# Performance work log

Hardware: AMD Instinct MI355X
Metric: run time of the kernel (lower is better)

The kernel has to match this reference:

```python
import jax, jax.numpy as jnp
import numpy as np

N, T, D, H, E, ED = 4096, 16, 5, 128, 32768, 32

def _leaky(x):
    return jnp.where(x >= 0, x, 0.2 * x)

def _lstm(x, Wih, Whh, bih, bhh):
    # x: [N, T, D] -> hidden sequence [N, T, H]; PyTorch gate order i,f,g,o
    pre = jnp.einsum('ntd,gd->tng', x, Wih) + bih + bhh  # [T, N, 4H]
    Hd = Whh.shape[1]
    def step(carry, p):
        h, c = carry
        g = p + h @ Whh.T
        i, f, gg, o = jnp.split(g, 4, axis=-1)
        c = jax.nn.sigmoid(f) * c + jax.nn.sigmoid(i) * jnp.tanh(gg)
        h = jax.nn.sigmoid(o) * jnp.tanh(c)
        return (h, c), h
    z = jnp.zeros((x.shape[0], Hd), x.dtype)
    _, hs = jax.lax.scan(step, (z, z), pre)
    return jnp.swapaxes(hs, 0, 1)

def _sire(x, src, dst, efeat, Wq, bq, Wk, bk, We, be, Wr, br):
    # SIREConv with agg_type='sum': m = LeakyReLU(eq[dst]+ek[src]+e); sum over in-edges; then linear_relation
    eq = x @ Wq.T + bq            # [N, T, H]
    ek = x @ Wk.T + bk            # [N, T, H]
    e = efeat @ We.T + be         # [E, H]
    m = _leaky(eq[dst] + ek[src] + e[:, None, :])  # [E, T, H]
    ft = jax.ops.segment_sum(m, dst, num_segments=x.shape[0])  # [N, T, H]
    return ft @ Wr.T + br

def _forward(stock_features, srcs, dsts, efeats, sire_ps, lstm_p, attn_p, mlp_p):
    sf = stock_features / jnp.mean(stock_features, axis=1, keepdims=True)
    sr = _lstm(sf, *lstm_p)  # [N, T, H]
    outs = [sr]
    for s, d, ef, p in zip(srcs, dsts, efeats, sire_ps):
        outs.append(_sire(sr, s, d, ef, *p))
    cat = jnp.concatenate(outs, axis=-1)  # [N, T, 4H]
    aw = jax.nn.softmax(cat @ attn_p[0].T + attn_p[1], axis=-2)  # softmax over time
    pooled = jnp.sum(cat * aw, axis=-2)   # [N, 4H]
    W1, b1, W2, b2 = mlp_p
    h = _leaky(pooled @ W1.T + b1)
    out = _leaky(h @ W2.T + b2)           # [N, 1]
    return out / sf[:, -1, 0:1] - 1.0


def setup_inputs() -> dict:
    key = jax.random.key(0)
    ks = iter(jax.random.split(key, 64))
    def nrm(shape, s=0.05):
        return jax.random.normal(next(ks), shape, jnp.float32) * s
    inp = {}
    inp['stock_features'] = jax.random.uniform(next(ks), (N, T, D), jnp.float32) + 0.5
    for g in ['wiki', 'industry', 'corr']:
        inp[g + '_src'] = jax.random.randint(next(ks), (E,), 0, N, jnp.int32)
        inp[g + '_dst'] = jax.random.randint(next(ks), (E,), 0, N, jnp.int32)
        inp[g + '_efeat'] = nrm((E, ED), 1.0)
        inp[g + '_Wq'] = nrm((H, H)); inp[g + '_bq'] = nrm((H,))
        inp[g + '_Wk'] = nrm((H, H)); inp[g + '_bk'] = nrm((H,))
        inp[g + '_We'] = nrm((H, ED)); inp[g + '_be'] = nrm((H,))
        inp[g + '_Wr'] = nrm((H, H)); inp[g + '_br'] = nrm((H,))
    inp['lstm_Wih'] = nrm((4 * H, D)); inp['lstm_Whh'] = nrm((4 * H, H))
    inp['lstm_bih'] = nrm((4 * H,)); inp['lstm_bhh'] = nrm((4 * H,))
    inp['attn_W'] = nrm((1, 4 * H)); inp['attn_b'] = nrm((1,))
    inp['mlp_W1'] = nrm((H, 4 * H)); inp['mlp_b1'] = nrm((H,))
    inp['mlp_W2'] = nrm((1, H)); inp['mlp_b2'] = nrm((1,))
    return inp


def reference(stock_features, wiki_src, wiki_dst, wiki_efeat,
              wiki_Wq, wiki_bq, wiki_Wk, wiki_bk, wiki_We, wiki_be, wiki_Wr, wiki_br,
              industry_src, industry_dst, industry_efeat,
              industry_Wq, industry_bq, industry_Wk, industry_bk, industry_We, industry_be, industry_Wr, industry_br,
              corr_src, corr_dst, corr_efeat,
              corr_Wq, corr_bq, corr_Wk, corr_bk, corr_We, corr_be, corr_Wr, corr_br,
              lstm_Wih, lstm_Whh, lstm_bih, lstm_bhh,
              attn_W, attn_b, mlp_W1, mlp_b1, mlp_W2, mlp_b2):
    srcs = (wiki_src, industry_src, corr_src)
    dsts = (wiki_dst, industry_dst, corr_dst)
    efeats = (wiki_efeat, industry_efeat, corr_efeat)
    sire_ps = ((wiki_Wq, wiki_bq, wiki_Wk, wiki_bk, wiki_We, wiki_be, wiki_Wr, wiki_br),
               (industry_Wq, industry_bq, industry_Wk, industry_bk, industry_We, industry_be, industry_Wr, industry_br),
               (corr_Wq, corr_bq, corr_Wk, corr_bk, corr_We, corr_be, corr_Wr, corr_br))
    return _forward(stock_features, srcs, dsts, efeats, sire_ps,
                    (lstm_Wih, lstm_Whh, lstm_bih, lstm_bhh),
                    (attn_W, attn_b), (mlp_W1, mlp_b1, mlp_W2, mlp_b2))
```

## Files before the change

### kernel.cpp

```cpp
#include <hip/hip_runtime.h>
#include <cstdint>
#include <cstddef>

#define NS 4096
#define TS 16
#define DF 5
#define HD 128
#define EE 32768
#define EDD 32

typedef __attribute__((ext_vector_type(8))) short bf16x8;
typedef __attribute__((ext_vector_type(4))) float f32x4;

__device__ __forceinline__ float sigmoidf_(float x){ return 1.f/(1.f+__expf(-x)); }
__device__ __forceinline__ float tanhf_(float x){ return 1.f - 2.f/(1.f+__expf(2.f*x)); }
__device__ __forceinline__ float leaky_(float x){ return x >= 0.f ? x : 0.2f*x; }

__device__ __forceinline__ unsigned short f2bf(float x){
  unsigned u = __float_as_uint(x);
  u += 0x7FFF + ((u>>16)&1);
  return (unsigned short)(u>>16);
}
__device__ __forceinline__ unsigned packbf(float a, float b){
  return (unsigned)f2bf(a) | ((unsigned)f2bf(b)<<16);
}
__device__ __forceinline__ void unpack2(unsigned u, float& a, float& b){
  a = __uint_as_float(u<<16);
  b = __uint_as_float(u & 0xFFFF0000u);
}
__device__ __forceinline__ void unpack8(uint4 q, float* f){
  unpack2(q.x, f[0], f[1]); unpack2(q.y, f[2], f[3]);
  unpack2(q.z, f[4], f[5]); unpack2(q.w, f[6], f[7]);
}
__device__ __forceinline__ bf16x8 ld_bf8(const unsigned short* p){
  union { uint4 u; bf16x8 v; } x; x.u = *(const uint4*)p; return x.v;
}

struct GemmB {
  const void* A[6];
  const float* B[6];
  const float* bias[6];
  void* C[6];
};
struct P3 { const int* p[3]; };

__global__ void k_sf(const float* __restrict__ x, float* __restrict__ sf){
  int id = blockIdx.x*256 + threadIdx.x;
  if (id >= NS*DF) return;
  int n = id / DF, d = id % DF;
  const float* xp = x + (size_t)n*TS*DF + d;
  float s = 0.f;
  #pragma unroll
  for (int t=0;t<TS;t++) s += xp[t*DF];
  float inv = (float)TS / s;
  float* sp = sf + (size_t)n*TS*DF + d;
  #pragma unroll
  for (int t=0;t<TS;t++) sp[t*DF] = xp[t*DF]*inv;
}

__global__ void k_cvt(const float* __restrict__ a, unsigned short* __restrict__ b, int n){
  int i = blockIdx.x*256 + threadIdx.x;
  if (i < n) b[i] = f2bf(a[i]);
}

__global__ __launch_bounds__(256,2)
void k_lstm(const float* __restrict__ sf, const unsigned short* __restrict__ WhhB,
            const float* __restrict__ Wih, const float* __restrict__ bih,
            const float* __restrict__ bhh, unsigned short* __restrict__ cat)
{
  __shared__ unsigned short hbuf[8*136];
  __shared__ float gates[8*516];
  __shared__ float sfb[8*80];
  int tid = threadIdx.x;
  int n0 = blockIdx.x * 8;
  int wv = tid>>6, lane = tid&63, lm = lane&15, lq = lane>>4;

  bf16x8 bfr[8][4];
  #pragma unroll
  for (int nt=0;nt<8;nt++){
    int g = wv*128 + nt*16 + lm;
    #pragma unroll
    for (int kt=0;kt<4;kt++)
      bfr[nt][kt] = *(const bf16x8*)&WhhB[g*128 + kt*32 + lq*8];
  }

  int j = tid & 127;
  int rbase = tid >> 7;
  float wih[4][5]; float bsum[4];
  #pragma unroll
  for (int gi=0; gi<4; gi++){
    int gc = gi*128 + j;
    #pragma unroll
    for (int d=0; d<5; d++) wih[gi][d] = Wih[gc*5+d];
    bsum[gi] = bih[gc] + bhh[gc];
  }
  float cst[4] = {0.f,0.f,0.f,0.f};

  for (int i=tid;i<8*136;i+=256) hbuf[i] = 0;
  for (int i=tid;i<8*80;i+=256) sfb[i] = sf[(size_t)n0*80 + i];
  __syncthreads();

  bf16x8 zf = {0,0,0,0,0,0,0,0};
  for (int t=0;t<16;t++){
    bf16x8 af[4];
    #pragma unroll
    for (int kt=0;kt<4;kt++)
      af[kt] = (lm < 8) ? *(const bf16x8*)&hbuf[lm*136 + kt*32 + lq*8] : zf;
    #pragma unroll
    for (int nt=0;nt<8;nt++){
      f32x4 acc = {0.f,0.f,0.f,0.f};
      #pragma unroll
      for (int kt=0;kt<4;kt++)
        acc = __builtin_amdgcn_mfma_f32_16x16x32_bf16(af[kt], bfr[nt][kt], acc, 0,0,0);
      if (lq < 2){
        int col = wv*128 + nt*16 + lm;
        #pragma unroll
        for (int i=0;i<4;i++)
          gates[(lq*4+i)*516 + col] = acc[i];
      }
    }
    __syncthreads();
    #pragma unroll
    for (int q=0;q<4;q++){
      int r = rbase + 2*q;
      const float* s = &sfb[r*80 + t*5];
      float pre[4];
      #pragma unroll
      for (int gi=0;gi<4;gi++){
        float a = bsum[gi];
        #pragma unroll
        for (int d=0;d<5;d++) a = fmaf(s[d], wih[gi][d], a);
        pre[gi] = a + gates[r*516 + gi*128 + j];
      }
      float iv = sigmoidf_(pre[0]);
      float fv = sigmoidf_(pre[1]);
      float gv = tanhf_(pre[2]);
      float ov = sigmoidf_(pre[3]);
      float c = fv*cst[q] + iv*gv;
      cst[q] = c;
      float h = ov*tanhf_(c);
      unsigned short hb = f2bf(h);
      hbuf[r*136 + j] = hb;
      cat[(size_t)((n0+r)*16 + t)*512 + j] = hb;
    }
    __syncthreads();
  }
}

template<int ABF, int CBF>
__global__ __launch_bounds__(256)
void gemm_mfma_b(GemmB gb, int lda, int ldb, int ldc, int K, int act)
{
  __shared__ unsigned short Asb[128*40];
  __shared__ unsigned short Bsb[128*40];
  int proj = blockIdx.x;
  size_t m0 = (size_t)blockIdx.y * 128;
  const float* Bp = gb.B[proj];
  const float* bp = gb.bias[proj];
  int tid = threadIdx.x;
  int wv = tid>>6, lane = tid&63, lm = lane&15, lq = lane>>4;

  f32x4 acc[2][8];
  #pragma unroll
  for (int mt=0;mt<2;mt++)
    #pragma unroll
    for (int nt=0;nt<8;nt++)
      acc[mt][nt] = (f32x4){0.f,0.f,0.f,0.f};

  for (int k0=0; k0<K; k0+=32){
    if (ABF){
      const unsigned short* A = (const unsigned short*)gb.A[proj];
      #pragma unroll
      for (int rep=0;rep<2;rep++){
        int idx = tid + rep*256;
        int row = idx>>2, c8 = idx&3;
        *(uint4*)&Asb[row*40 + c8*8] = *(const uint4*)&A[(m0+row)*(size_t)lda + k0 + c8*8];
      }
    } else {
      const float* A = (const float*)gb.A[proj];
      #pragma unroll
      for (int rep=0;rep<4;rep++){
        int idx = tid + rep*256;
        int row = idx>>3, c4 = idx&7;
        float4 a = *(const float4*)&A[(m0+row)*(size_t)lda + k0 + c4*4];
        *(uint2*)&Asb[row*40 + c4*4] = make_uint2(packbf(a.x,a.y), packbf(a.z,a.w));
      }
    }
    #pragma unroll
    for (int rep=0;rep<4;rep++){
      int idx = tid + rep*256;
      int row = idx>>3, c4 = idx&7;
      float4 b = *(const float4*)&Bp[(size_t)row*ldb + k0 + c4*4];
      *(uint2*)&Bsb[row*40 + c4*4] = make_uint2(packbf(b.x,b.y), packbf(b.z,b.w));
    }
    __syncthreads();
    bf16x8 afr[2], bfr[8];
    #pragma unroll
    for (int mt=0;mt<2;mt++)
      afr[mt] = ld_bf8(&Asb[(wv*32 + mt*16 + lm)*40 + lq*8]);
    #pragma unroll
    for (int nt=0;nt<8;nt++)
      bfr[nt] = ld_bf8(&Bsb[(nt*16 + lm)*40 + lq*8]);
    #pragma unroll
    for (int mt=0;mt<2;mt++)
      #pragma unroll
      for (int nt=0;nt<8;nt++)
        acc[mt][nt] = __builtin_amdgcn_mfma_f32_16x16x32_bf16(afr[mt], bfr[nt], acc[mt][nt], 0,0,0);
    __syncthreads();
  }

  #pragma unroll
  for (int mt=0;mt<2;mt++){
    #pragma unroll
    for (int nt=0;nt<8;nt++){
      int col = nt*16 + lm;
      float bv = bp[col];
      #pragma unroll
      for (int i=0;i<4;i++){
        float o = acc[mt][nt][i] + bv;
        if (act) o = leaky_(o);
        size_t ridx = (m0 + wv*32 + mt*16 + lq*4 + i)*(size_t)ldc + col;
        if (CBF) ((unsigned short*)gb.C[proj])[ridx] = f2bf(o);
        else     ((float*)gb.C[proj])[ridx] = o;
      }
    }
  }
}

__global__ void k_zero_i(int* p, int n){ int i=blockIdx.x*256+threadIdx.x; if(i<n) p[i]=0; }

__global__ void k_count(P3 dst, int* __restrict__ cnt){
  int e = blockIdx.x*256+threadIdx.x;
  int g = blockIdx.y;
  atomicAdd(&cnt[g*4096 + dst.p[g][e]], 1);
}

__global__ __launch_bounds__(1024)
void k_scan(const int* __restrict__ cnt_, int* __restrict__ rs_, int* __restrict__ woff_){
  __shared__ int buf[1024];
  int g = blockIdx.x;
  const int* cnt = cnt_ + g*4096;
  int* rs = rs_ + g*4097;
  int* woff = woff_ + g*4096;
  int tid = threadIdx.x;
  int b = tid*4;
  int v0=cnt[b],v1=cnt[b+1],v2=cnt[b+2],v3=cnt[b+3];
  int s = v0+v1+v2+v3;
  buf[tid]=s;
  __syncthreads();
  for (int off=1; off<1024; off<<=1){
    int t = (tid>=off) ? buf[tid-off] : 0;
    __syncthreads();
    buf[tid] += t;
    __syncthreads();
  }
  int excl = buf[tid] - s;
  rs[b+0]=excl; woff[b+0]=excl; excl+=v0;
  rs[b+1]=excl; woff[b+1]=excl; excl+=v1;
  rs[b+2]=excl; woff[b+2]=excl; excl+=v2;
  rs[b+3]=excl; woff[b+3]=excl;
  if (tid==1023) rs[4096]=excl+v3;
}

__global__ void k_fill(P3 dst, int* __restrict__ woff, int* __restrict__ eidx){
  int e = blockIdx.x*256+threadIdx.x;
  int g = blockIdx.y;
  int pos = atomicAdd(&woff[g*4096 + dst.p[g][e]], 1);
  eidx[g*EE + pos] = e;
}

__global__ __launch_bounds__(256)
void k_edge(const unsigned short* __restrict__ eqk, const unsigned short* __restrict__ eeb,
            P3 src, const int* __restrict__ rs_, const int* __restrict__ eidx_,
            unsigned short* __restrict__ ft_)
{
  int n = blockIdx.x;
  int g = blockIdx.y;
  const unsigned short* eqb = eqk + (size_t)(2*g)  *NS*TS*128;
  const unsigned short* ekb = eqk + (size_t)(2*g+1)*NS*TS*128;
  const unsigned short* eeg = eeb + (size_t)g*EE*128;
  unsigned short* ft = ft_ + (size_t)g*NS*TS*128;
  const int* srcp = src.p[g];
  const int* rs = rs_ + g*4097;
  const int* eidx = eidx_ + g*EE;
  int tid = threadIdx.x;
  int t = tid>>4, hb = (tid&15)*8;
  size_t own = ((size_t)(n*16+t))*128 + hb;
  float eqv[8], acc[8];
  unpack8(*(const uint4*)&eqb[own], eqv);
  #pragma unroll
  for (int j=0;j<8;j++) acc[j]=0.f;
  int i0 = rs[n], i1 = rs[n+1];
  for (int i=i0;i<i1;i++){
    int e = eidx[i];
    int s = srcp[e];
    uint4 kq = *(const uint4*)&ekb[((size_t)(s*16+t))*128 + hb];
    uint4 eq4 = *(const uint4*)&eeg[(size_t)e*128 + hb];
    float kf[8], ef[8];
    unpack8(kq, kf); unpack8(eq4, ef);
    #pragma unroll
    for (int j=0;j<8;j++)
      acc[j] += leaky_(eqv[j] + kf[j] + ef[j]);
  }
  uint4 o;
  o.x = packbf(acc[0],acc[1]); o.y = packbf(acc[2],acc[3]);
  o.z = packbf(acc[4],acc[5]); o.w = packbf(acc[6],acc[7]);
  *(uint4*)&ft[own] = o;
}

__global__ __launch_bounds__(256)
void k_attn(const unsigned short* __restrict__ cat, const float* __restrict__ attnW,
            const float* __restrict__ attnB, unsigned short* __restrict__ pooled)
{
  __shared__ unsigned short ct[16*512];
  __shared__ float sred[4][16];
  int n = blockIdx.x, tid = threadIdx.x;
  {
    const uint4* srcp = (const uint4*)(cat + (size_t)n*8192);
    uint4* dstp = (uint4*)ct;
    for (int i=tid;i<1024;i+=256) dstp[i] = srcp[i];
  }
  __syncthreads();
  int c0 = tid*2;
  float w0 = attnW[c0], w1 = attnW[c0+1];
  const unsigned* ctu = (const unsigned*)ct;
  float loc[16];
  #pragma unroll
  for (int t=0;t<16;t++){
    float a,b; unpack2(ctu[t*256 + tid], a, b);
    loc[t] = a*w0 + b*w1;
  }
  #pragma unroll
  for (int t=0;t<16;t++){
    float v = loc[t];
    for (int off=1; off<64; off<<=1) v += __shfl_xor(v, off, 64);
    loc[t]=v;
  }
  int wave = tid >> 6, lane = tid & 63;
  if (lane==0){
    #pragma unroll
    for (int t=0;t<16;t++) sred[wave][t]=loc[t];
  }
  __syncthreads();
  float s[16]; float m=-1e30f;
  float ab = attnB[0];
  #pragma unroll
  for (int t=0;t<16;t++){ s[t] = sred[0][t]+sred[1][t]+sred[2][t]+sred[3][t] + ab; m = fmaxf(m, s[t]); }
  float sum=0.f;
  #pragma unroll
  for (int t=0;t<16;t++){ s[t] = __expf(s[t]-m); sum += s[t]; }
  float inv = 1.f/sum;
  float p0=0.f,p1=0.f;
  #pragma unroll
  for (int t=0;t<16;t++){
    float a = s[t]*inv;
    float x,y; unpack2(ctu[t*256 + tid], x, y);
    p0 = fmaf(x, a, p0); p1 = fmaf(y, a, p1);
  }
  ((unsigned*)pooled)[(size_t)n*256 + tid] = packbf(p0,p1);
}

__global__ __launch_bounds__(256)
void k_final(const float* __restrict__ hmlp, const float* __restrict__ W2,
             const float* __restrict__ b2, const float* __restrict__ sf,
             float* __restrict__ out)
{
  int tid = threadIdx.x;
  int n = blockIdx.x*4 + (tid>>6);
  int lane = tid & 63;
  const float* hp = hmlp + (size_t)n*128;
  float v = hp[lane]*W2[lane] + hp[64+lane]*W2[64+lane];
  for (int off=1; off<64; off<<=1) v += __shfl_xor(v, off, 64);
  if (lane==0){
    float o = v + b2[0];
    o = leaky_(o);
    out[n] = o / sf[(size_t)n*80 + 75] - 1.f;
  }
}

extern "C" void kernel_launch(void* const* d_in, const int* in_sizes, int n_in,
                              void* d_out, int out_size, void* d_ws, size_t ws_size,
                              hipStream_t stream)
{
  const float* x    = (const float*)d_in[0];
  const float* Wih  = (const float*)d_in[34];
  const float* Whh  = (const float*)d_in[35];
  const float* bih  = (const float*)d_in[36];
  const float* bhh  = (const float*)d_in[37];
  const float* attnW= (const float*)d_in[38];
  const float* attnB= (const float*)d_in[39];
  const float* W1   = (const float*)d_in[40];
  const float* b1   = (const float*)d_in[41];
  const float* W2   = (const float*)d_in[42];
  const float* b2   = (const float*)d_in[43];

  char* w = (char*)d_ws;
  size_t o = 0;
  unsigned short* cat    = (unsigned short*)(w+o); o += (size_t)NS*TS*512*2;
  unsigned short* eqk    = (unsigned short*)(w+o); o += (size_t)6*NS*TS*128*2;
  unsigned short* eeb    = (unsigned short*)(w+o); o += (size_t)3*EE*128*2;
  unsigned short* ft     = (unsigned short*)(w+o); o += (size_t)3*NS*TS*128*2;
  unsigned short* pooled = (unsigned short*)(w+o); o += (size_t)NS*512*2;
  float* sf   = (float*)(w+o); o += (size_t)NS*TS*DF*4;
  float* hmlp = (float*)(w+o); o += (size_t)NS*HD*4;
  unsigned short* whhB = (unsigned short*)(w+o); o += (size_t)512*128*2;
  int* cnt  = (int*)(w+o); o += 3*4096*4;
  int* rs   = (int*)(w+o); o += 3*4097*4;
  int* woff = (int*)(w+o); o += 3*4096*4;
  int* eidx = (int*)(w+o); o += (size_t)3*EE*4;

  P3 dsts = {{ (const int*)d_in[2], (const int*)d_in[13], (const int*)d_in[24] }};
  P3 srcs = {{ (const int*)d_in[1], (const int*)d_in[12], (const int*)d_in[23] }};

  k_sf <<<80, 256, 0, stream>>>(x, sf);
  k_cvt<<<256, 256, 0, stream>>>(Whh, whhB, 512*128);
  k_lstm<<<512, 256, 0, stream>>>(sf, whhB, Wih, bih, bhh, cat);

  k_zero_i<<<48, 256, 0, stream>>>(cnt, 3*4096);
  k_count <<<dim3(EE/256,3), 256, 0, stream>>>(dsts, cnt);
  k_scan  <<<3, 1024, 0, stream>>>(cnt, rs, woff);
  k_fill  <<<dim3(EE/256,3), 256, 0, stream>>>(dsts, woff, eidx);

  {
    GemmB gb;
    for (int g=0; g<3; g++){
      int base = 1 + g*11;
      gb.A[2*g] = cat;   gb.A[2*g+1] = cat;
      gb.B[2*g]    = (const float*)d_in[base+3];
      gb.bias[2*g] = (const float*)d_in[base+4];
      gb.B[2*g+1]    = (const float*)d_in[base+5];
      gb.bias[2*g+1] = (const float*)d_in[base+6];
      gb.C[2*g]   = eqk + (size_t)(2*g)  *NS*TS*128;
      gb.C[2*g+1] = eqk + (size_t)(2*g+1)*NS*TS*128;
    }
    gemm_mfma_b<1,1><<<dim3(6,512), 256, 0, stream>>>(gb, 512, 128, 128, 128, 0);
  }
  {
    GemmB gb;
    for (int g=0; g<3; g++){
      int base = 1 + g*11;
      gb.A[g]    = (const float*)d_in[base+2];
      gb.B[g]    = (const float*)d_in[base+7];
      gb.bias[g] = (const float*)d_in[base+8];
      gb.C[g]    = eeb + (size_t)g*EE*128;
    }
    gemm_mfma_b<0,1><<<dim3(3,EE/128), 256, 0, stream>>>(gb, 32, 32, 128, 32, 0);
  }

  k_edge<<<dim3(NS,3), 256, 0, stream>>>(eqk, eeb, srcs, rs, eidx, ft);

  {
    GemmB gb;
    for (int g=0; g<3; g++){
      int base = 1 + g*11;
      gb.A[g]    = ft + (size_t)g*NS*TS*128;
      gb.B[g]    = (const float*)d_in[base+9];
      gb.bias[g] = (const float*)d_in[base+10];
      gb.C[g]    = cat + (size_t)(1+g)*128;
    }
    gemm_mfma_b<1,1><<<dim3(3,512), 256, 0, stream>>>(gb, 128, 128, 512, 128, 0);
  }

  k_attn<<<NS, 256, 0, stream>>>(cat, attnW, attnB, pooled);
  {
    GemmB gb;
    gb.A[0] = pooled; gb.B[0] = W1; gb.bias[0] = b1; gb.C[0] = hmlp;
    gemm_mfma_b<1,0><<<dim3(1,32), 256, 0, stream>>>(gb, 512, 512, 128, 512, 1);
  }
  k_final<<<NS/4, 256, 0, stream>>>(hmlp, W2, b2, sf, (float*)d_out);
}
```

Measured before the change: 434.4 us.

## Merge independent stages into multi-role kernels and retile edge aggregation grid

Independent small kernels are combined into block-range dispatched mega-kernels. One kernel does sf normalization, Whh conversion and count zeroing. A second runs the LSTM alongside the edge-feature GEMM and in-degree counting, and a third runs the q/k projection GEMM alongside the CSR fill. The aim is to cut launch count and let the LSTM's low-occupancy tail overlap with unrelated work. k_edge is also regridded to one block per 16 nodes per timestep. The shared launch bounds and shared-memory size may hurt occupancy for the GEMM roles, and atomics now interleave with heavy compute.

Measured after the change: 416.0 us. 4.2% less time.

```diff
diff --git a/kernel.cpp b/kernel.cpp
--- a/kernel.cpp
+++ b/kernel.cpp
@@ -36,43 +36,92 @@
   union { uint4 u; bf16x8 v; } x; x.u = *(const uint4*)p; return x.v;
 }
 
-struct GemmB {
-  const void* A[6];
-  const float* B[6];
-  const float* bias[6];
-  void* C[6];
-};
-struct P3 { const int* p[3]; };
-
-__global__ void k_sf(const float* __restrict__ x, float* __restrict__ sf){
-  int id = blockIdx.x*256 + threadIdx.x;
-  if (id >= NS*DF) return;
-  int n = id / DF, d = id % DF;
-  const float* xp = x + (size_t)n*TS*DF + d;
-  float s = 0.f;
-  #pragma unroll
-  for (int t=0;t<TS;t++) s += xp[t*DF];
-  float inv = (float)TS / s;
-  float* sp = sf + (size_t)n*TS*DF + d;
-  #pragma unroll
-  for (int t=0;t<TS;t++) sp[t*DF] = xp[t*DF]*inv;
-}
-
-__global__ void k_cvt(const float* __restrict__ a, unsigned short* __restrict__ b, int n){
-  int i = blockIdx.x*256 + threadIdx.x;
-  if (i < n) b[i] = f2bf(a[i]);
-}
-
-__global__ __launch_bounds__(256,2)
-void k_lstm(const float* __restrict__ sf, const unsigned short* __restrict__ WhhB,
-            const float* __restrict__ Wih, const float* __restrict__ bih,
-            const float* __restrict__ bhh, unsigned short* __restrict__ cat)
-{
-  __shared__ unsigned short hbuf[8*136];
-  __shared__ float gates[8*516];
-  __shared__ float sfb[8*80];
+template<int ABF, int CBF>
+__device__ __forceinline__ void gemm_dev(const void* Av, int lda,
+    const float* __restrict__ Bp, int ldb, const float* __restrict__ bp,
+    void* Cv, int ldc, int K, int act, size_t m0,
+    unsigned short* Asb, unsigned short* Bsb)
+{
   int tid = threadIdx.x;
-  int n0 = blockIdx.x * 8;
+  int wv = tid>>6, lane = tid&63, lm = lane&15, lq = lane>>4;
+  f32x4 acc[2][8];
+  #pragma unroll
+  for (int mt=0;mt<2;mt++)
+    #pragma unroll
+    for (int nt=0;nt<8;nt++)
+      acc[mt][nt] = (f32x4){0.f,0.f,0.f,0.f};
+
+  for (int k0=0; k0<K; k0+=32){
+    if (ABF){
+      const unsigned short* A = (const unsigned short*)Av;
+      #pragma unroll
+      for (int rep=0;rep<2;rep++){
+        int idx = tid + rep*256;
+        int row = idx>>2, c8 = idx&3;
+        *(uint4*)&Asb[row*40 + c8*8] = *(const uint4*)&A[(m0+row)*(size_t)lda + k0 + c8*8];
+      }
+    } else {
+      const float* A = (const float*)Av;
+      #pragma unroll
+      for (int rep=0;rep<4;rep++){
+        int idx = tid + rep*256;
+        int row = idx>>3, c4 = idx&7;
+        float4 a = *(const float4*)&A[(m0+row)*(size_t)lda + k0 + c4*4];
+        *(uint2*)&Asb[row*40 + c4*4] = make_uint2(packbf(a.x,a.y), packbf(a.z,a.w));
+      }
+    }
+    #pragma unroll
+    for (int rep=0;rep<4;rep++){
+      int idx = tid + rep*256;
+      int row = idx>>3, c4 = idx&7;
+      float4 b = *(const float4*)&Bp[(size_t)row*ldb + k0 + c4*4];
+      *(uint2*)&Bsb[row*40 + c4*4] = make_uint2(packbf(b.x,b.y), packbf(b.z,b.w));
+    }
+    __syncthreads();
+    bf16x8 afr[2], bfr[8];
+    #pragma unroll
+    for (int mt=0;mt<2;mt++)
+      afr[mt] = ld_bf8(&Asb[(wv*32 + mt*16 + lm)*40 + lq*8]);
+    #pragma unroll
+    for (int nt=0;nt<8;nt++)
+      bfr[nt] = ld_bf8(&Bsb[(nt*16 + lm)*40 + lq*8]);
+    #pragma unroll
+    for (int mt=0;mt<2;mt++)
+      #pragma unroll
+      for (int nt=0;nt<8;nt++)
+        acc[mt][nt] = __builtin_amdgcn_mfma_f32_16x16x32_bf16(afr[mt], bfr[nt], acc[mt][nt], 0,0,0);
+    __syncthreads();
+  }
+
+  #pragma unroll
+  for (int mt=0;mt<2;mt++){
+    #pragma unroll
+    for (int nt=0;nt<8;nt++){
+      int col = nt*16 + lm;
+      float bv = bp[col];
+      #pragma unroll
+      for (int i=0;i<4;i++){
+        float o = acc[mt][nt][i] + bv;
+        if (act) o = leaky_(o);
+        size_t ridx = (m0 + wv*32 + mt*16 + lq*4 + i)*(size_t)ldc + col;
+        if (CBF) ((unsigned short*)Cv)[ridx] = f2bf(o);
+        else     ((float*)Cv)[ridx] = o;
+      }
+    }
+  }
+}
+
+__device__ void lstm8_dev(int blk, const float* __restrict__ sf,
+                          const unsigned short* __restrict__ WhhB,
+                          const float* __restrict__ Wih, const float* __restrict__ bih,
+                          const float* __restrict__ bhh, unsigned short* __restrict__ cat,
+                          char* smem)
+{
+  float* gates = (float*)smem;
+  unsigned short* hbuf = (unsigned short*)(smem+16512);
+  float* sfb = (float*)(smem+16512+2176);
+  int tid = threadIdx.x;
+  int n0 = blk*8;
   int wv = tid>>6, lane = tid&63, lm = lane&15, lq = lane>>4;
 
   bf16x8 bfr[8][4];
@@ -85,7 +134,7 @@
   }
 
   int j = tid & 127;
-  int rbase = tid >> 7;
+  int rb = tid >> 7;
   float wih[4][5]; float bsum[4];
   #pragma unroll
   for (int gi=0; gi<4; gi++){
@@ -96,8 +145,8 @@
   }
   float cst[4] = {0.f,0.f,0.f,0.f};
 
-  for (int i=tid;i<8*136;i+=256) hbuf[i] = 0;
-  for (int i=tid;i<8*80;i+=256) sfb[i] = sf[(size_t)n0*80 + i];
+  for (int i=tid;i<544;i+=256) ((unsigned*)hbuf)[i] = 0;
+  for (int i=tid;i<640;i+=256) sfb[i] = sf[(size_t)n0*80 + i];
   __syncthreads();
 
   bf16x8 zf = {0,0,0,0,0,0,0,0};
@@ -122,7 +171,7 @@
     __syncthreads();
     #pragma unroll
     for (int q=0;q<4;q++){
-      int r = rbase + 2*q;
+      int r = rb + 2*q;
       const float* s = &sfb[r*80 + t*5];
       float pre[4];
       #pragma unroll
@@ -139,100 +188,71 @@
       float c = fv*cst[q] + iv*gv;
       cst[q] = c;
       float h = ov*tanhf_(c);
-      unsigned short hb = f2bf(h);
-      hbuf[r*136 + j] = hb;
-      cat[(size_t)((n0+r)*16 + t)*512 + j] = hb;
+      unsigned short hb16 = f2bf(h);
+      hbuf[r*136 + j] = hb16;
+      cat[(size_t)((n0+r)*16 + t)*512 + j] = hb16;
     }
     __syncthreads();
   }
 }
 
-template<int ABF, int CBF>
-__global__ __launch_bounds__(256)
-void gemm_mfma_b(GemmB gb, int lda, int ldb, int ldc, int K, int act)
-{
-  __shared__ unsigned short Asb[128*40];
-  __shared__ unsigned short Bsb[128*40];
-  int proj = blockIdx.x;
-  size_t m0 = (size_t)blockIdx.y * 128;
-  const float* Bp = gb.B[proj];
-  const float* bp = gb.bias[proj];
-  int tid = threadIdx.x;
-  int wv = tid>>6, lane = tid&63, lm = lane&15, lq = lane>>4;
-
-  f32x4 acc[2][8];
-  #pragma unroll
-  for (int mt=0;mt<2;mt++)
-    #pragma unroll
-    for (int nt=0;nt<8;nt++)
-      acc[mt][nt] = (f32x4){0.f,0.f,0.f,0.f};
-
-  for (int k0=0; k0<K; k0+=32){
-    if (ABF){
-      const unsigned short* A = (const unsigned short*)gb.A[proj];
-      #pragma unroll
-      for (int rep=0;rep<2;rep++){
-        int idx = tid + rep*256;
-        int row = idx>>2, c8 = idx&3;
-        *(uint4*)&Asb[row*40 + c8*8] = *(const uint4*)&A[(m0+row)*(size_t)lda + k0 + c8*8];
-      }
-    } else {
-      const float* A = (const float*)gb.A[proj];
-      #pragma unroll
-      for (int rep=0;rep<4;rep++){
-        int idx = tid + rep*256;
-        int row = idx>>3, c4 = idx&7;
-        float4 a = *(const float4*)&A[(m0+row)*(size_t)lda + k0 + c4*4];
-        *(uint2*)&Asb[row*40 + c4*4] = make_uint2(packbf(a.x,a.y), packbf(a.z,a.w));
-      }
-    }
-    #pragma unroll
-    for (int rep=0;rep<4;rep++){
-      int idx = tid + rep*256;
-      int row = idx>>3, c4 = idx&7;
-      float4 b = *(const float4*)&Bp[(size_t)row*ldb + k0 + c4*4];
-      *(uint2*)&Bsb[row*40 + c4*4] = make_uint2(packbf(b.x,b.y), packbf(b.z,b.w));
-    }
-    __syncthreads();
-    bf16x8 afr[2], bfr[8];
-    #pragma unroll
-    for (int mt=0;mt<2;mt++)
-      afr[mt] = ld_bf8(&Asb[(wv*32 + mt*16 + lm)*40 + lq*8]);
-    #pragma unroll
-    for (int nt=0;nt<8;nt++)
-      bfr[nt] = ld_bf8(&Bsb[(nt*16 + lm)*40 + lq*8]);
-    #pragma unroll
-    for (int mt=0;mt<2;mt++)
-      #pragma unroll
-      for (int nt=0;nt<8;nt++)
-        acc[mt][nt] = __builtin_amdgcn_mfma_f32_16x16x32_bf16(afr[mt], bfr[nt], acc[mt][nt], 0,0,0);
-    __syncthreads();
-  }
-
-  #pragma unroll
-  for (int mt=0;mt<2;mt++){
-    #pragma unroll
-    for (int nt=0;nt<8;nt++){
-      int col = nt*16 + lm;
-      float bv = bp[col];
-      #pragma unroll
-      for (int i=0;i<4;i++){
-        float o = acc[mt][nt][i] + bv;
-        if (act) o = leaky_(o);
-        size_t ridx = (m0 + wv*32 + mt*16 + lq*4 + i)*(size_t)ldc + col;
-        if (CBF) ((unsigned short*)gb.C[proj])[ridx] = f2bf(o);
-        else     ((float*)gb.C[proj])[ridx] = o;
-      }
-    }
-  }
-}
-
-__global__ void k_zero_i(int* p, int n){ int i=blockIdx.x*256+threadIdx.x; if(i<n) p[i]=0; }
-
-__global__ void k_count(P3 dst, int* __restrict__ cnt){
-  int e = blockIdx.x*256+threadIdx.x;
-  int g = blockIdx.y;
-  atomicAdd(&cnt[g*4096 + dst.p[g][e]], 1);
+__global__ __launch_bounds__(256)
+void k_prolog(const float* __restrict__ x, float* __restrict__ sf,
+              const float* __restrict__ Whh, unsigned short* __restrict__ whhB,
+              int* __restrict__ cnt)
+{
+  int b = blockIdx.x, tid = threadIdx.x;
+  if (b < 80){
+    int id = b*256 + tid;
+    if (id < NS*DF){
+      int n = id / DF, d = id % DF;
+      const float* xp = x + (size_t)n*TS*DF + d;
+      float s = 0.f;
+      #pragma unroll
+      for (int t=0;t<TS;t++) s += xp[t*DF];
+      float inv = (float)TS / s;
+      float* sp = sf + (size_t)n*TS*DF + d;
+      #pragma unroll
+      for (int t=0;t<TS;t++) sp[t*DF] = xp[t*DF]*inv;
+    }
+  } else if (b < 336){
+    int i = (b-80)*256 + tid;
+    whhB[i] = f2bf(Whh[i]);
+  } else {
+    int i = (b-336)*256 + tid;
+    cnt[i] = 0;
+  }
+}
+
+struct M1 {
+  const float *sf, *Wih, *bih, *bhh;
+  const unsigned short* WhhB;
+  unsigned short* cat;
+  const float *ef[3]; const float *We[3]; const float *be[3];
+  unsigned short* eeb;
+  const int* dst[3];
+  int* cnt;
+};
+__global__ __launch_bounds__(256,2)
+void k_mega1(M1 p)
+{
+  __shared__ __align__(16) char smem[21504];
+  int b = blockIdx.x;
+  if (b < 512){
+    lstm8_dev(b, p.sf, p.WhhB, p.Wih, p.bih, p.bhh, p.cat, smem);
+  } else if (b < 1280){
+    int idx = b - 512;
+    int proj = idx % 3, mt = idx / 3;
+    unsigned short* Asb = (unsigned short*)smem;
+    unsigned short* Bsb = Asb + 128*40;
+    gemm_dev<0,1>(p.ef[proj], 32, p.We[proj], 32, p.be[proj],
+                  p.eeb + (size_t)proj*EE*128, 128, 32, 0, (size_t)mt*128, Asb, Bsb);
+  } else {
+    int idx = b - 1280;
+    int g = idx >> 7, blk = idx & 127;
+    int e = blk*256 + threadIdx.x;
+    atomicAdd(&p.cnt[g*4096 + p.dst[g][e]], 1);
+  }
 }
 
 __global__ __launch_bounds__(1024)
@@ -262,20 +282,39 @@
   if (tid==1023) rs[4096]=excl+v3;
 }
 
-__global__ void k_fill(P3 dst, int* __restrict__ woff, int* __restrict__ eidx){
-  int e = blockIdx.x*256+threadIdx.x;
-  int g = blockIdx.y;
-  int pos = atomicAdd(&woff[g*4096 + dst.p[g][e]], 1);
-  eidx[g*EE + pos] = e;
-}
-
+struct M2 {
+  const unsigned short* cat;
+  const float* W[6]; const float* bias[6];
+  unsigned short* eqk;
+  const int* dst[3];
+  int* woff; int* eidx;
+};
+__global__ __launch_bounds__(256)
+void k_mega2(M2 p)
+{
+  __shared__ __align__(16) unsigned short Asb[128*40];
+  __shared__ __align__(16) unsigned short Bsb[128*40];
+  int b = blockIdx.x;
+  if (b < 3072){
+    int proj = b % 6, mt = b / 6;
+    gemm_dev<1,1>(p.cat, 512, p.W[proj], 128, p.bias[proj],
+                  p.eqk + (size_t)proj*NS*TS*128, 128, 128, 0, (size_t)mt*128, Asb, Bsb);
+  } else {
+    int idx = b - 3072;
+    int g = idx >> 7, blk = idx & 127;
+    int e = blk*256 + threadIdx.x;
+    int pos = atomicAdd(&p.woff[g*4096 + p.dst[g][e]], 1);
+    p.eidx[g*EE + pos] = e;
+  }
+}
+
+struct P3 { const int* p[3]; };
 __global__ __launch_bounds__(256)
 void k_edge(const unsigned short* __restrict__ eqk, const unsigned short* __restrict__ eeb,
             P3 src, const int* __restrict__ rs_, const int* __restrict__ eidx_,
             unsigned short* __restrict__ ft_)
 {
-  int n = blockIdx.x;
-  int g = blockIdx.y;
+  int nb = blockIdx.x, t = blockIdx.y, g = blockIdx.z;
   const unsigned short* eqb = eqk + (size_t)(2*g)  *NS*TS*128;
   const unsigned short* ekb = eqk + (size_t)(2*g+1)*NS*TS*128;
   const unsigned short* eeg = eeb + (size_t)g*EE*128;
@@ -284,7 +323,8 @@
   const int* rs = rs_ + g*4097;
   const int* eidx = eidx_ + g*EE;
   int tid = threadIdx.x;
-  int t = tid>>4, hb = (tid&15)*8;
+  int n = nb*16 + (tid>>4);
+  int hb = (tid&15)*8;
   size_t own = ((size_t)(n*16+t))*128 + hb;
   float eqv[8], acc[8];
   unpack8(*(const uint4*)&eqb[own], eqv);
@@ -308,6 +348,22 @@
   *(uint4*)&ft[own] = o;
 }
 
+struct WrP {
+  const unsigned short* A[3];
+  const float* B[3]; const float* bias[3];
+  unsigned short* C[3];
+};
+__global__ __launch_bounds__(256)
+void k_wr(WrP p)
+{
+  __shared__ __align__(16) unsigned short Asb[128*40];
+  __shared__ __align__(16) unsigned short Bsb[128*40];
+  int proj = blockIdx.x;
+  size_t m0 = (size_t)blockIdx.y * 128;
+  gemm_dev<1,1>(p.A[proj], 128, p.B[proj], 128, p.bias[proj],
+                p.C[proj], 512, 128, 0, m0, Asb, Bsb);
+}
+
 __global__ __launch_bounds__(256)
 void k_attn(const unsigned short* __restrict__ cat, const float* __restrict__ attnW,
             const float* __restrict__ attnB, unsigned short* __restrict__ pooled)
@@ -358,6 +414,16 @@
     p0 = fmaf(x, a, p0); p1 = fmaf(y, a, p1);
   }
   ((unsigned*)pooled)[(size_t)n*256 + tid] = packbf(p0,p1);
+}
+
+__global__ __launch_bounds__(256)
+void k_mlp(const unsigned short* __restrict__ pooled, const float* __restrict__ W1,
+           const float* __restrict__ b1, float* __restrict__ hmlp)
+{
+  __shared__ __align__(16) unsigned short Asb[128*40];
+  __shared__ __align__(16) unsigned short Bsb[128*40];
+  gemm_dev<1,0>(pooled, 512, W1, 512, b1, hmlp, 128, 512, 1,
+                (size_t)blockIdx.x*128, Asb, Bsb);
 }
 
 __global__ __launch_bounds__(256)
@@ -409,63 +475,55 @@
   int* woff = (int*)(w+o); o += 3*4096*4;
   int* eidx = (int*)(w+o); o += (size_t)3*EE*4;
 
-  P3 dsts = {{ (const int*)d_in[2], (const int*)d_in[13], (const int*)d_in[24] }};
   P3 srcs = {{ (const int*)d_in[1], (const int*)d_in[12], (const int*)d_in[23] }};
 
-  k_sf <<<80, 256, 0, stream>>>(x, sf);
-  k_cvt<<<256, 256, 0, stream>>>(Whh, whhB, 512*128);
-  k_lstm<<<512, 256, 0, stream>>>(sf, whhB, Wih, bih, bhh, cat);
-
-  k_zero_i<<<48, 256, 0, stream>>>(cnt, 3*4096);
-  k_count <<<dim3(EE/256,3), 256, 0, stream>>>(dsts, cnt);
-  k_scan  <<<3, 1024, 0, stream>>>(cnt, rs, woff);
-  k_fill  <<<dim3(EE/256,3), 256, 0, stream>>>(dsts, woff, eidx);
+  k_prolog<<<384, 256, 0, stream>>>(x, sf, Whh, whhB, cnt);
 
   {
-    GemmB gb;
+    M1 p;
+    p.sf = sf; p.Wih = Wih; p.bih = bih; p.bhh = bhh;
+    p.WhhB = whhB; p.cat = cat; p.eeb = eeb; p.cnt = cnt;
     for (int g=0; g<3; g++){
       int base = 1 + g*11;
-      gb.A[2*g] = cat;   gb.A[2*g+1] = cat;
-      gb.B[2*g]    = (const float*)d_in[base+3];
-      gb.bias[2*g] = (const float*)d_in[base+4];
-      gb.B[2*g+1]    = (const float*)d_in[base+5];
-      gb.bias[2*g+1] = (const float*)d_in[base+6];
-      gb.C[2*g]   = eqk + (size_t)(2*g)  *NS*TS*128;
-      gb.C[2*g+1] = eqk + (size_t)(2*g+1)*NS*TS*128;
-    }
-    gemm_mfma_b<1,1><<<dim3(6,512), 256, 0, stream>>>(gb, 512, 128, 128, 128, 0);
-  }
+      p.ef[g] = (const float*)d_in[base+2];
+      p.We[g] = (const float*)d_in[base+7];
+      p.be[g] = (const float*)d_in[base+8];
+      p.dst[g] = (const int*)d_in[base+1];
+    }
+    k_mega1<<<1664, 256, 0, stream>>>(p);
+  }
+
+  k_scan<<<3, 1024, 0, stream>>>(cnt, rs, woff);
+
   {
-    GemmB gb;
+    M2 p;
+    p.cat = cat; p.eqk = eqk; p.woff = woff; p.eidx = eidx;
     for (int g=0; g<3; g++){
       int base = 1 + g*11;
-      gb.A[g]    = (const float*)d_in[base+2];
-      gb.B[g]    = (const float*)d_in[base+7];
-      gb.bias[g] = (const float*)d_in[base+8];
-      gb.C[g]    = eeb + (size_t)g*EE*128;
-    }
-    gemm_mfma_b<0,1><<<dim3(3,EE/128), 256, 0, stream>>>(gb, 32, 32, 128, 32, 0);
-  }
-
-  k_edge<<<dim3(NS,3), 256, 0, stream>>>(eqk, eeb, srcs, rs, eidx, ft);
+      p.W[2*g]      = (const float*)d_in[base+3];
+      p.bias[2*g]   = (const float*)d_in[base+4];
+      p.W[2*g+1]    = (const float*)d_in[base+5];
+      p.bias[2*g+1] = (const float*)d_in[base+6];
+      p.dst[g] = (const int*)d_in[base+1];
+    }
+    k_mega2<<<3456, 256, 0, stream>>>(p);
+  }
+
+  k_edge<<<dim3(256,16,3), 256, 0, stream>>>(eqk, eeb, srcs, rs, eidx, ft);
 
   {
-    GemmB gb;
+    WrP p;
     for (int g=0; g<3; g++){
       int base = 1 + g*11;
-      gb.A[g]    = ft + (size_t)g*NS*TS*128;
-      gb.B[g]    = (const float*)d_in[base+9];
-      gb.bias[g] = (const float*)d_in[base+10];
-      gb.C[g]    = cat + (size_t)(1+g)*128;
-    }
-    gemm_mfma_b<1,1><<<dim3(3,512), 256, 0, stream>>>(gb, 128, 128, 512, 128, 0);
+      p.A[g]    = ft + (size_t)g*NS*TS*128;
+      p.B[g]    = (const float*)d_in[base+9];
+      p.bias[g] = (const float*)d_in[base+10];
+      p.C[g]    = cat + (size_t)(1+g)*128;
+    }
+    k_wr<<<dim3(3,512), 256, 0, stream>>>(p);
   }
 
   k_attn<<<NS, 256, 0, stream>>>(cat, attnW, attnB, pooled);
-  {
-    GemmB gb;
-    gb.A[0] = pooled; gb.B[0] = W1; gb.bias[0] = b1; gb.C[0] = hmlp;
-    gemm_mfma_b<1,0><<<dim3(1,32), 256, 0, stream>>>(gb, 512, 512, 128, 512, 1);
-  }
+  k_mlp<<<32, 256, 0, stream>>>(pooled, W1, b1, hmlp);
   k_final<<<NS/4, 256, 0, stream>>>(hmlp, W2, b2, sf, (float*)d_out);
 }
```
